# Kernel tuning notes

Measured on AMD Instinct MI355X. Metric: run time of the kernel, lower is better.

The kernel has to match this reference:

```python
import jax, jax.numpy as jnp
import numpy as np

TOPK = 64  # topk_atoms
EPS = 1e-9


def setup_inputs() -> dict:
    key = jax.random.key(0)
    k1, k2 = jax.random.split(key)
    B, N = 32, 2048          # batch, num_atoms
    C, R = 64, 32            # channels, rank of low-rank factors U
    accumulated = jax.random.normal(k1, (B, N), dtype=jnp.float32)
    U = jax.random.normal(k2, (C, N, R), dtype=jnp.float32)
    return {"accumulated": accumulated, "U": U}


def reference(accumulated, U):
    # accumulated: [B, N]; U: [C, N, R]
    B, N = accumulated.shape
    C, _, R = U.shape
    K = min(TOPK, N)

    # ---- CoActivationComputer._compute: per-row top-k ----
    topk_vals, topk_idx = jax.lax.top_k(accumulated, K)  # [B,K], [B,K]

    # ---- CoActState.frob_inner_lowrank(U) ----
    U_t = jnp.transpose(U, (1, 2, 0))        # [N, R, C]
    U_topk = U_t[topk_idx]                   # [B, K, R, C] irregular gather
    Au = jnp.einsum('bk,bkrc->brc', topk_vals, U_topk)  # [B, R, C]
    frob = (Au ** 2).sum(axis=1) / (K * R + EPS)        # [B, C]

    # ---- CoActState.to_dense(): scatter_add of rank-1 outer products ----
    vals = topk_vals[:, :, None] * topk_vals[:, None, :]           # [B, K, K]
    flat_idx = (topk_idx[:, :, None] * N + topk_idx[:, None, :])   # [B, K, K]
    flat_idx = flat_idx.reshape(B, K * K)
    M = jnp.zeros((B, N * N), dtype=accumulated.dtype)
    M = M.at[jnp.arange(B)[:, None], flat_idx].add(vals.reshape(B, K * K))
    M = M.reshape(B, N, N)

    return topk_vals, topk_idx, frob, M
```

## Files before the change

### kernel.cpp

```cpp
#include <hip/hip_runtime.h>

#define B 32
#define N 2048
#define K 64
#define C 64
#define R 32

__device__ __forceinline__ unsigned long long kmax(unsigned long long a, unsigned long long b) {
    return a > b ? a : b;
}

__global__ __launch_bounds__(256) void topk_kernel(const float* __restrict__ acc,
                                                   float* __restrict__ out_vals,
                                                   float* __restrict__ out_idxf,
                                                   float* __restrict__ ws_vals,
                                                   int* __restrict__ ws_idx) {
    __shared__ unsigned long long wmax[4];
    const int t = threadIdx.x;
    const int b = blockIdx.x;
    const int lane = t & 63;
    const int wave = t >> 6;
    const float* row = acc + b * N;

    unsigned long long kr[8];
    unsigned long long m = 0ull;
#pragma unroll
    for (int j = 0; j < 8; ++j) {
        int i = t + 256 * j;
        unsigned int bits = __float_as_uint(row[i]);
        unsigned int u = (bits & 0x80000000u) ? ~bits : (bits | 0x80000000u);
        kr[j] = ((unsigned long long)u << 32) | (unsigned int)(N - 1 - i);
        m = kmax(m, kr[j]);
    }

    for (int s = 0; s < K; ++s) {
        unsigned long long w = m;
#pragma unroll
        for (int off = 32; off; off >>= 1)
            w = kmax(w, __shfl_down(w, off, 64));
        if (lane == 0) wmax[wave] = w;
        __syncthreads();
        unsigned long long best = kmax(kmax(wmax[0], wmax[1]), kmax(wmax[2], wmax[3]));
        if (t == 0) {
            unsigned int u = (unsigned int)(best >> 32);
            unsigned int bits = (u & 0x80000000u) ? (u ^ 0x80000000u) : ~u;
            float v = __uint_as_float(bits);
            int idx = (N - 1) - (int)(best & 0xFFFFFFFFull);
            out_vals[b * K + s] = v;
            out_idxf[b * K + s] = (float)idx;
            ws_vals[b * K + s] = v;
            ws_idx[b * K + s] = idx;
        }
        if (m == best) {
            unsigned long long nm = 0ull;
#pragma unroll
            for (int j = 0; j < 8; ++j) {
                if (kr[j] == best) kr[j] = 0ull;
                nm = kmax(nm, kr[j]);
            }
            m = nm;
        }
        __syncthreads();
    }
}

__global__ __launch_bounds__(256) void frob_kernel(const float* __restrict__ U,
                                                   const float* __restrict__ ws_vals,
                                                   const int* __restrict__ ws_idx,
                                                   float* __restrict__ out_frob) {
    __shared__ float sv[K];
    __shared__ int si[K];
    const int t = threadIdx.x;
    const int b = blockIdx.x >> 3;
    const int cg = blockIdx.x & 7;
    if (t < K) {
        sv[t] = ws_vals[b * K + t];
        si[t] = ws_idx[b * K + t];
    }
    __syncthreads();
    const int r = t & 31;
    const int c = (cg << 3) + (t >> 5);
    const float* Uc = U + (size_t)c * (N * R) + r;
    float acc = 0.0f;
#pragma unroll 8
    for (int k = 0; k < K; ++k)
        acc = fmaf(sv[k], Uc[(size_t)si[k] * R], acc);
    float x = acc * acc;
#pragma unroll
    for (int off = 16; off; off >>= 1)
        x += __shfl_xor(x, off, 32);
    if (r == 0) out_frob[b * C + c] = x * (1.0f / 2048.0f);
}

#define ROWS_PER_BLOCK 8
__global__ __launch_bounds__(256) void dense_kernel(const float* __restrict__ ws_vals,
                                                    const int* __restrict__ ws_idx,
                                                    float* __restrict__ M) {
    __shared__ float sv[K];
    __shared__ int si[K];
    __shared__ int match[ROWS_PER_BLOCK];
    const int t = threadIdx.x;
    const int b = blockIdx.x >> 8;
    const int rowblk = blockIdx.x & 255;
    const int row0 = rowblk * ROWS_PER_BLOCK;

    if (t < K) {
        sv[t] = ws_vals[b * K + t];
        si[t] = ws_idx[b * K + t];
    }
    if (t < ROWS_PER_BLOCK) match[t] = -1;
    __syncthreads();
    if (t < K) {
        int d = si[t] - row0;
        if (d >= 0 && d < ROWS_PER_BLOCK) match[d] = t;
    }

    float* base = M + ((size_t)b << 22) + ((size_t)row0 << 11);
    float4* b4 = (float4*)base;
    const float4 z = make_float4(0.f, 0.f, 0.f, 0.f);
#pragma unroll
    for (int j = 0; j < 16; ++j)
        b4[t + 256 * j] = z;

    __syncthreads();

#pragma unroll
    for (int rr = 0; rr < ROWS_PER_BLOCK; ++rr) {
        int p = match[rr];
        if (p >= 0 && t < K) {
            base[(size_t)rr * N + si[t]] = sv[p] * sv[t];
        }
    }
}

extern "C" void kernel_launch(void* const* d_in, const int* in_sizes, int n_in,
                              void* d_out, int out_size, void* d_ws, size_t ws_size,
                              hipStream_t stream) {
    const float* acc = (const float*)d_in[0];
    const float* U = (const float*)d_in[1];
    float* out = (float*)d_out;

    float* out_vals = out;
    float* out_idxf = out + B * K;
    float* out_frob = out + 2 * B * K;
    float* out_M = out + 3 * B * K;

    float* ws_vals = (float*)d_ws;
    int* ws_idx = (int*)((char*)d_ws + B * K * sizeof(float));

    topk_kernel<<<B, 256, 0, stream>>>(acc, out_vals, out_idxf, ws_vals, ws_idx);
    frob_kernel<<<B * 8, 256, 0, stream>>>(U, ws_vals, ws_idx, out_frob);
    dense_kernel<<<B * (N / ROWS_PER_BLOCK), 256, 0, stream>>>(ws_vals, ws_idx, out_M);
}
```

Baseline: 579.9 us.

## Overlap dense-matrix zeroing with top-k and fuse scatter into frob kernel

Zero-filling the 512MB dense output now runs in extra blocks of the top-k launch, so it no longer waits for the top-k result. The scatter of outer products moves into extra blocks of the frob kernel, one block per batch writing all K*K entries directly. The zero stores use nontemporal hints to avoid polluting cache. This removes one kernel launch and the serial dependency of zeroing on top-k, at the cost of scattered single-float writes and reliance on kernel ordering for correctness.

```diff
diff --git a/kernel.cpp b/kernel.cpp
--- a/kernel.cpp
+++ b/kernel.cpp
@@ -6,17 +6,36 @@
 #define C 64
 #define R 32
 
+typedef float vf4 __attribute__((ext_vector_type(4)));
+
 __device__ __forceinline__ unsigned long long kmax(unsigned long long a, unsigned long long b) {
     return a > b ? a : b;
 }
 
-__global__ __launch_bounds__(256) void topk_kernel(const float* __restrict__ acc,
-                                                   float* __restrict__ out_vals,
-                                                   float* __restrict__ out_idxf,
-                                                   float* __restrict__ ws_vals,
-                                                   int* __restrict__ ws_idx) {
+#define ROWS_PER_BLOCK 8
+#define ZERO_BLOCKS (B * (N / ROWS_PER_BLOCK))
+
+__global__ __launch_bounds__(256) void fused_topk_zero_kernel(const float* __restrict__ acc,
+                                                              float* __restrict__ out_vals,
+                                                              float* __restrict__ out_idxf,
+                                                              float* __restrict__ ws_vals,
+                                                              int* __restrict__ ws_idx,
+                                                              float* __restrict__ M) {
+    const int t = threadIdx.x;
+
+    if (blockIdx.x >= B) {
+        const int zb = blockIdx.x - B;
+        const int b = zb >> 8;
+        const int rowblk = zb & 255;
+        vf4* b4 = (vf4*)(M + ((size_t)b << 22) + ((size_t)rowblk << 14));
+        const vf4 z = {0.f, 0.f, 0.f, 0.f};
+#pragma unroll
+        for (int j = 0; j < 16; ++j)
+            __builtin_nontemporal_store(z, &b4[t + 256 * j]);
+        return;
+    }
+
     __shared__ unsigned long long wmax[4];
-    const int t = threadIdx.x;
     const int b = blockIdx.x;
     const int lane = t & 63;
     const int wave = t >> 6;
@@ -64,13 +83,35 @@
     }
 }
 
-__global__ __launch_bounds__(256) void frob_kernel(const float* __restrict__ U,
-                                                   const float* __restrict__ ws_vals,
-                                                   const int* __restrict__ ws_idx,
-                                                   float* __restrict__ out_frob) {
+__global__ __launch_bounds__(256) void fused_frob_scatter_kernel(const float* __restrict__ U,
+                                                                 const float* __restrict__ ws_vals,
+                                                                 const int* __restrict__ ws_idx,
+                                                                 float* __restrict__ out_frob,
+                                                                 float* __restrict__ M) {
+    const int t = threadIdx.x;
+
+    if (blockIdx.x >= B * 8) {
+        __shared__ float sv[K];
+        __shared__ int si[K];
+        const int b = blockIdx.x - B * 8;
+        if (t < K) {
+            sv[t] = ws_vals[b * K + t];
+            si[t] = ws_idx[b * K + t];
+        }
+        __syncthreads();
+        float* Mb = M + ((size_t)b << 22);
+#pragma unroll
+        for (int q = 0; q < 16; ++q) {
+            int p = q * 256 + t;
+            int i = p >> 6;
+            int j = p & 63;
+            Mb[(size_t)si[i] * N + si[j]] = sv[i] * sv[j];
+        }
+        return;
+    }
+
     __shared__ float sv[K];
     __shared__ int si[K];
-    const int t = threadIdx.x;
     const int b = blockIdx.x >> 3;
     const int cg = blockIdx.x & 7;
     if (t < K) {
@@ -81,56 +122,15 @@
     const int r = t & 31;
     const int c = (cg << 3) + (t >> 5);
     const float* Uc = U + (size_t)c * (N * R) + r;
-    float acc = 0.0f;
+    float accv = 0.0f;
 #pragma unroll 8
     for (int k = 0; k < K; ++k)
-        acc = fmaf(sv[k], Uc[(size_t)si[k] * R], acc);
-    float x = acc * acc;
+        accv = fmaf(sv[k], Uc[(size_t)si[k] * R], accv);
+    float x = accv * accv;
 #pragma unroll
     for (int off = 16; off; off >>= 1)
         x += __shfl_xor(x, off, 32);
     if (r == 0) out_frob[b * C + c] = x * (1.0f / 2048.0f);
-}
-
-#define ROWS_PER_BLOCK 8
-__global__ __launch_bounds__(256) void dense_kernel(const float* __restrict__ ws_vals,
-                                                    const int* __restrict__ ws_idx,
-                                                    float* __restrict__ M) {
-    __shared__ float sv[K];
-    __shared__ int si[K];
-    __shared__ int match[ROWS_PER_BLOCK];
-    const int t = threadIdx.x;
-    const int b = blockIdx.x >> 8;
-    const int rowblk = blockIdx.x & 255;
-    const int row0 = rowblk * ROWS_PER_BLOCK;
-
-    if (t < K) {
-        sv[t] = ws_vals[b * K + t];
-        si[t] = ws_idx[b * K + t];
-    }
-    if (t < ROWS_PER_BLOCK) match[t] = -1;
-    __syncthreads();
-    if (t < K) {
-        int d = si[t] - row0;
-        if (d >= 0 && d < ROWS_PER_BLOCK) match[d] = t;
-    }
-
-    float* base = M + ((size_t)b << 22) + ((size_t)row0 << 11);
-    float4* b4 = (float4*)base;
-    const float4 z = make_float4(0.f, 0.f, 0.f, 0.f);
-#pragma unroll
-    for (int j = 0; j < 16; ++j)
-        b4[t + 256 * j] = z;
-
-    __syncthreads();
-
-#pragma unroll
-    for (int rr = 0; rr < ROWS_PER_BLOCK; ++rr) {
-        int p = match[rr];
-        if (p >= 0 && t < K) {
-            base[(size_t)rr * N + si[t]] = sv[p] * sv[t];
-        }
-    }
 }
 
 extern "C" void kernel_launch(void* const* d_in, const int* in_sizes, int n_in,
@@ -148,7 +148,8 @@
     float* ws_vals = (float*)d_ws;
     int* ws_idx = (int*)((char*)d_ws + B * K * sizeof(float));
 
-    topk_kernel<<<B, 256, 0, stream>>>(acc, out_vals, out_idxf, ws_vals, ws_idx);
-    frob_kernel<<<B * 8, 256, 0, stream>>>(U, ws_vals, ws_idx, out_frob);
-    dense_kernel<<<B * (N / ROWS_PER_BLOCK), 256, 0, stream>>>(ws_vals, ws_idx, out_M);
+    fused_topk_zero_kernel<<<B + ZERO_BLOCKS, 256, 0, stream>>>(acc, out_vals, out_idxf,
+                                                                ws_vals, ws_idx, out_M);
+    fused_frob_scatter_kernel<<<B * 8 + B, 256, 0, stream>>>(U, ws_vals, ws_idx,
+                                                             out_frob, out_M);
 }
```

After: 563.1 us. 2.9% less time.
